# Optimization experiments

Hardware: AMD Instinct MI355X
Metric: run time of the kernel (lower is better)

Reference implementation:

```python
import jax, jax.numpy as jnp
import numpy as np

N_NODES = 100000
N_EDGES = 1000000

def _gcn_conv(x, W, b, src, dst, n_nodes):
    # PyG GCNConv: linear first, then symmetric-normalized aggregation with self loops
    x = x @ W  # [N, F_out]
    loop = jnp.arange(n_nodes, dtype=src.dtype)
    src2 = jnp.concatenate([src, loop])
    dst2 = jnp.concatenate([dst, loop])
    deg = jax.ops.segment_sum(jnp.ones(src2.shape[0], x.dtype), dst2, num_segments=n_nodes)
    dinv = jnp.where(deg > 0, jax.lax.rsqrt(deg), 0.0)
    norm = dinv[src2] * dinv[dst2]  # [E+N]
    msgs = x[src2] * norm[:, None]  # gather + scale
    out = jax.ops.segment_sum(msgs, dst2, num_segments=n_nodes)  # scatter-add
    return out + b

def _pair_norm_si(x):
    # mode 'PN-SI', scale=1
    x = x - x.mean(axis=0)
    row_norm = jnp.sqrt(1e-6 + jnp.sum(x * x, axis=1, keepdims=True))
    return x / row_norm

def setup_inputs() -> dict:
    key = jax.random.key(0)
    k1, k2, k3, k4 = jax.random.split(key, 4)
    in_c, hid_c, out_c = 256, 64, 40
    x = jax.random.normal(k1, (N_NODES, in_c), dtype=jnp.float32)
    edge_index = jax.random.randint(k2, (2, N_EDGES), 0, N_NODES, dtype=jnp.int64)
    W1 = jax.random.normal(k3, (in_c, hid_c), dtype=jnp.float32) / np.sqrt(in_c)
    b1 = jnp.zeros((hid_c,), jnp.float32)
    W2 = jax.random.normal(k4, (hid_c, out_c), dtype=jnp.float32) / np.sqrt(hid_c)
    b2 = jnp.zeros((out_c,), jnp.float32)
    return {"x": x, "edge_index": edge_index, "W1": W1, "b1": b1, "W2": W2, "b2": b2}

def reference(x, edge_index, W1, b1, W2, b2):
    src, dst = edge_index[0], edge_index[1]
    n = x.shape[0]
    h = jax.nn.relu(_gcn_conv(x, W1, b1, src, dst, n))
    h = _gcn_conv(h, W2, b2, src, dst, n)
    h = _pair_norm_si(h)
    return jax.nn.log_softmax(h, axis=1)
```

## Files before the change

### kernel.cpp

```cpp
#include <hip/hip_runtime.h>
#include <hip/hip_fp16.h>
#include <math.h>

#define F_IN  256
#define F_HID 64
#define F_OUT 40
#define HS2_LD 64

typedef _Float16 h8 __attribute__((ext_vector_type(8)));
typedef _Float16 h4 __attribute__((ext_vector_type(4)));
typedef float f4 __attribute__((ext_vector_type(4)));

__global__ void k_deg(const int* __restrict__ dst, unsigned* __restrict__ degc, int E) {
    int i = blockIdx.x * blockDim.x + threadIdx.x;
    if (i < E) atomicAdd(&degc[dst[i]], 1u);
}

__global__ __launch_bounds__(256) void k_scanA(const unsigned* __restrict__ degc,
                                               unsigned* __restrict__ exscan,
                                               unsigned* __restrict__ bsum, int N) {
    __shared__ unsigned s[256];
    int tid = threadIdx.x;
    int i = blockIdx.x * 256 + tid;
    unsigned v = (i < N) ? degc[i] : 0u;
    s[tid] = v;
    __syncthreads();
    for (int off = 1; off < 256; off <<= 1) {
        unsigned t = (tid >= off) ? s[tid - off] : 0u;
        __syncthreads();
        s[tid] += t;
        __syncthreads();
    }
    if (i < N) exscan[i] = s[tid] - v;
    if (tid == 255) bsum[blockIdx.x] = s[255];
}

__global__ __launch_bounds__(512) void k_scanB(unsigned* __restrict__ bsum, int nb) {
    __shared__ unsigned s[512];
    int tid = threadIdx.x;
    unsigned v = (tid < nb) ? bsum[tid] : 0u;
    s[tid] = v;
    __syncthreads();
    for (int off = 1; off < 512; off <<= 1) {
        unsigned t = (tid >= off) ? s[tid - off] : 0u;
        __syncthreads();
        s[tid] += t;
        __syncthreads();
    }
    if (tid < nb) bsum[tid] = s[tid] - v;
}

__global__ void k_scanC(const unsigned* __restrict__ degc, const unsigned* __restrict__ exscan,
                        const unsigned* __restrict__ bsum, unsigned* __restrict__ rowptr,
                        float* __restrict__ dinv, int N, int E) {
    int i = blockIdx.x * blockDim.x + threadIdx.x;
    if (i < N) {
        rowptr[i] = exscan[i] + bsum[i >> 8];
        dinv[i] = rsqrtf((float)degc[i] + 1.0f);
        if (i == 0) rowptr[N] = (unsigned)E;
    }
}

__global__ void k_fill(const int* __restrict__ src, const int* __restrict__ dst,
                       const unsigned* __restrict__ rowptr, unsigned* __restrict__ cursor,
                       unsigned* __restrict__ col, int E) {
    int e = blockIdx.x * blockDim.x + threadIdx.x;
    if (e >= E) return;
    int d = dst[e];
    unsigned p = atomicAdd(&cursor[d], 1u);
    col[rowptr[d] + p] = (unsigned)src[e];
}

__global__ void k_wt(const float* __restrict__ W1, __half* __restrict__ Wt) {
    int i = blockIdx.x * 256 + threadIdx.x;
    int k = i >> 6, n = i & 63;
    Wt[n * 256 + k] = __float2half(W1[i]);
}

#define XS 136
__global__ __launch_bounds__(256) void k_mm1(const float* __restrict__ x,
                                             const __half* __restrict__ Wth,
                                             const float* __restrict__ dinv,
                                             __half* __restrict__ hs1o, int N) {
    __shared__ _Float16 sX[64 * XS];
    const _Float16* Wt = (const _Float16*)Wth;
    _Float16* hs1 = (_Float16*)hs1o;
    int tid = threadIdx.x;
    int lane = tid & 63;
    int wv = tid >> 6;
    int m15 = lane & 15;
    int q = lane >> 4;
    int nbase = blockIdx.x * 64;

    h8 bf[8];
    #pragma unroll
    for (int kt = 0; kt < 8; ++kt)
        bf[kt] = *(const h8*)(Wt + (wv * 16 + m15) * 256 + kt * 32 + q * 8);

    f4 acc[4];
    #pragma unroll
    for (int mt = 0; mt < 4; ++mt) acc[mt] = (f4){0.f, 0.f, 0.f, 0.f};

    #pragma unroll
    for (int c = 0; c < 2; ++c) {
        #pragma unroll
        for (int p = 0; p < 8; ++p) {
            int idx = p * 256 + tid;
            int row = idx >> 5;
            int c4  = idx & 31;
            int node = nbase + row;
            float4 v = (node < N) ? *(const float4*)(x + (size_t)node * F_IN + c * 128 + c4 * 4)
                                  : make_float4(0.f, 0.f, 0.f, 0.f);
            h4 hv = { (_Float16)v.x, (_Float16)v.y, (_Float16)v.z, (_Float16)v.w };
            *(h4*)&sX[row * XS + c4 * 4] = hv;
        }
        __syncthreads();
        #pragma unroll
        for (int kt2 = 0; kt2 < 4; ++kt2) {
            #pragma unroll
            for (int mt = 0; mt < 4; ++mt) {
                h8 a = *(const h8*)&sX[(mt * 16 + m15) * XS + kt2 * 32 + q * 8];
                acc[mt] = __builtin_amdgcn_mfma_f32_16x16x32_f16(a, bf[c * 4 + kt2], acc[mt], 0, 0, 0);
            }
        }
        __syncthreads();
    }

    #pragma unroll
    for (int mt = 0; mt < 4; ++mt) {
        #pragma unroll
        for (int r = 0; r < 4; ++r) {
            int node = nbase + mt * 16 + q * 4 + r;
            if (node < N) {
                float din = dinv[node];
                hs1[(size_t)node * F_HID + wv * 16 + m15] = (_Float16)(acc[mt][r] * din);
            }
        }
    }
}

__global__ __launch_bounds__(256) void k_agg1(const unsigned* __restrict__ rowptr,
                                              const unsigned* __restrict__ col,
                                              const float* __restrict__ dinv,
                                              const __half* __restrict__ hs1,
                                              const float* __restrict__ bias1,
                                              float* __restrict__ agg1, int N) {
    int lane = threadIdx.x & 63;
    int w = blockIdx.x * 4 + (threadIdx.x >> 6);
    int na = 2 * w, nb = 2 * w + 1;
    if (na >= N) return;

    float dinA = dinv[na];
    unsigned aE = rowptr[na], aEnd = rowptr[na + 1];
    float accA = __half2float(hs1[(size_t)na * F_HID + lane]);

    bool hasB = (nb < N);
    float dinB = 0.f, accB = 0.f;
    unsigned bE = 0, bEnd = 0;
    if (hasB) {
        dinB = dinv[nb];
        bE = rowptr[nb]; bEnd = rowptr[nb + 1];
        accB = __half2float(hs1[(size_t)nb * F_HID + lane]);
    }

    while (aE + 4 <= aEnd && bE + 4 <= bEnd) {
        unsigned sa0 = col[aE], sa1 = col[aE + 1], sa2 = col[aE + 2], sa3 = col[aE + 3];
        unsigned sb0 = col[bE], sb1 = col[bE + 1], sb2 = col[bE + 2], sb3 = col[bE + 3];
        float va0 = __half2float(hs1[(size_t)sa0 * F_HID + lane]);
        float va1 = __half2float(hs1[(size_t)sa1 * F_HID + lane]);
        float va2 = __half2float(hs1[(size_t)sa2 * F_HID + lane]);
        float va3 = __half2float(hs1[(size_t)sa3 * F_HID + lane]);
        float vb0 = __half2float(hs1[(size_t)sb0 * F_HID + lane]);
        float vb1 = __half2float(hs1[(size_t)sb1 * F_HID + lane]);
        float vb2 = __half2float(hs1[(size_t)sb2 * F_HID + lane]);
        float vb3 = __half2float(hs1[(size_t)sb3 * F_HID + lane]);
        accA += (va0 + va1) + (va2 + va3);
        accB += (vb0 + vb1) + (vb2 + vb3);
        aE += 4; bE += 4;
    }
    while (aE + 4 <= aEnd) {
        unsigned s0 = col[aE], s1 = col[aE + 1], s2 = col[aE + 2], s3 = col[aE + 3];
        float v0 = __half2float(hs1[(size_t)s0 * F_HID + lane]);
        float v1 = __half2float(hs1[(size_t)s1 * F_HID + lane]);
        float v2 = __half2float(hs1[(size_t)s2 * F_HID + lane]);
        float v3 = __half2float(hs1[(size_t)s3 * F_HID + lane]);
        accA += (v0 + v1) + (v2 + v3);
        aE += 4;
    }
    while (bE + 4 <= bEnd) {
        unsigned s0 = col[bE], s1 = col[bE + 1], s2 = col[bE + 2], s3 = col[bE + 3];
        float v0 = __half2float(hs1[(size_t)s0 * F_HID + lane]);
        float v1 = __half2float(hs1[(size_t)s1 * F_HID + lane]);
        float v2 = __half2float(hs1[(size_t)s2 * F_HID + lane]);
        float v3 = __half2float(hs1[(size_t)s3 * F_HID + lane]);
        accB += (v0 + v1) + (v2 + v3);
        bE += 4;
    }
    while (aE < aEnd && bE < bEnd) {
        unsigned sa = col[aE], sb = col[bE];
        accA += __half2float(hs1[(size_t)sa * F_HID + lane]);
        accB += __half2float(hs1[(size_t)sb * F_HID + lane]);
        ++aE; ++bE;
    }
    while (aE < aEnd) { accA += __half2float(hs1[(size_t)col[aE] * F_HID + lane]); ++aE; }
    while (bE < bEnd) { accB += __half2float(hs1[(size_t)col[bE] * F_HID + lane]); ++bE; }

    float bv = bias1[lane];
    float vA = accA * dinA + bv;
    agg1[(size_t)na * F_HID + lane] = vA > 0.f ? vA : 0.f;
    if (hasB) {
        float vB = accB * dinB + bv;
        agg1[(size_t)nb * F_HID + lane] = vB > 0.f ? vB : 0.f;
    }
}

__global__ __launch_bounds__(320) void k_mm2(const float* __restrict__ a,
                                             const float* __restrict__ W2,
                                             const float* __restrict__ dinv,
                                             __half* __restrict__ hs2, int N) {
    __shared__ float sW[F_HID * F_OUT];
    int tid = threadIdx.x;
    for (int idx = tid; idx < F_HID * F_OUT; idx += 320) sW[idx] = W2[idx];
    __syncthreads();

    int f = tid % F_OUT, r = tid / F_OUT;
    int node = blockIdx.x * 8 + r;
    if (node >= N) return;
    const float* ar = a + (size_t)node * F_HID;
    float acc = 0.f;
    #pragma unroll 8
    for (int k = 0; k < F_HID; ++k) acc = fmaf(ar[k], sW[k * F_OUT + f], acc);
    hs2[(size_t)node * HS2_LD + f] = __float2half(acc * dinv[node]);
}

__global__ __launch_bounds__(256) void k_agg2(const unsigned* __restrict__ rowptr,
                                              const unsigned* __restrict__ col,
                                              const float* __restrict__ dinv,
                                              const __half* __restrict__ hs2,
                                              float* __restrict__ out,
                                              float* __restrict__ colsum, int N) {
    __shared__ float part[256];
    int lane = threadIdx.x & 63;
    int wid = threadIdx.x >> 6;
    int nwaves = gridDim.x * 4;
    float cacc = 0.f;
    if (lane < F_OUT) {
        for (int w = blockIdx.x * 4 + wid; 2 * w < N; w += nwaves) {
            int na = 2 * w, nb = 2 * w + 1;
            float dinA = dinv[na];
            unsigned aE = rowptr[na], aEnd = rowptr[na + 1];
            float accA = __half2float(hs2[(size_t)na * HS2_LD + lane]);
            bool hasB = (nb < N);
            float dinB = 0.f, accB = 0.f;
            unsigned bE = 0, bEnd = 0;
            if (hasB) {
                dinB = dinv[nb];
                bE = rowptr[nb]; bEnd = rowptr[nb + 1];
                accB = __half2float(hs2[(size_t)nb * HS2_LD + lane]);
            }

            while (aE + 4 <= aEnd && bE + 4 <= bEnd) {
                unsigned sa0 = col[aE], sa1 = col[aE + 1], sa2 = col[aE + 2], sa3 = col[aE + 3];
                unsigned sb0 = col[bE], sb1 = col[bE + 1], sb2 = col[bE + 2], sb3 = col[bE + 3];
                float va0 = __half2float(hs2[(size_t)sa0 * HS2_LD + lane]);
                float va1 = __half2float(hs2[(size_t)sa1 * HS2_LD + lane]);
                float va2 = __half2float(hs2[(size_t)sa2 * HS2_LD + lane]);
                float va3 = __half2float(hs2[(size_t)sa3 * HS2_LD + lane]);
                float vb0 = __half2float(hs2[(size_t)sb0 * HS2_LD + lane]);
                float vb1 = __half2float(hs2[(size_t)sb1 * HS2_LD + lane]);
                float vb2 = __half2float(hs2[(size_t)sb2 * HS2_LD + lane]);
                float vb3 = __half2float(hs2[(size_t)sb3 * HS2_LD + lane]);
                accA += (va0 + va1) + (va2 + va3);
                accB += (vb0 + vb1) + (vb2 + vb3);
                aE += 4; bE += 4;
            }
            while (aE + 4 <= aEnd) {
                unsigned s0 = col[aE], s1 = col[aE + 1], s2 = col[aE + 2], s3 = col[aE + 3];
                float v0 = __half2float(hs2[(size_t)s0 * HS2_LD + lane]);
                float v1 = __half2float(hs2[(size_t)s1 * HS2_LD + lane]);
                float v2 = __half2float(hs2[(size_t)s2 * HS2_LD + lane]);
                float v3 = __half2float(hs2[(size_t)s3 * HS2_LD + lane]);
                accA += (v0 + v1) + (v2 + v3);
                aE += 4;
            }
            while (bE + 4 <= bEnd) {
                unsigned s0 = col[bE], s1 = col[bE + 1], s2 = col[bE + 2], s3 = col[bE + 3];
                float v0 = __half2float(hs2[(size_t)s0 * HS2_LD + lane]);
                float v1 = __half2float(hs2[(size_t)s1 * HS2_LD + lane]);
                float v2 = __half2float(hs2[(size_t)s2 * HS2_LD + lane]);
                float v3 = __half2float(hs2[(size_t)s3 * HS2_LD + lane]);
                accB += (v0 + v1) + (v2 + v3);
                bE += 4;
            }
            while (aE < aEnd && bE < bEnd) {
                unsigned sa = col[aE], sb = col[bE];
                accA += __half2float(hs2[(size_t)sa * HS2_LD + lane]);
                accB += __half2float(hs2[(size_t)sb * HS2_LD + lane]);
                ++aE; ++bE;
            }
            while (aE < aEnd) { accA += __half2float(hs2[(size_t)col[aE] * HS2_LD + lane]); ++aE; }
            while (bE < bEnd) { accB += __half2float(hs2[(size_t)col[bE] * HS2_LD + lane]); ++bE; }

            accA *= dinA;
            out[(size_t)na * F_OUT + lane] = accA;
            cacc += accA;
            if (hasB) {
                accB *= dinB;
                out[(size_t)nb * F_OUT + lane] = accB;
                cacc += accB;
            }
        }
    }
    part[threadIdx.x] = cacc;
    __syncthreads();
    if (threadIdx.x < F_OUT) {
        float s = part[threadIdx.x] + part[64 + threadIdx.x] + part[128 + threadIdx.x] + part[192 + threadIdx.x];
        atomicAdd(&colsum[threadIdx.x], s);
    }
}

__global__ __launch_bounds__(128) void k_final(float* __restrict__ out,
                                               const float* __restrict__ colsum, int N) {
    __shared__ float sMean[F_OUT];
    if (threadIdx.x < F_OUT) sMean[threadIdx.x] = colsum[threadIdx.x] * (1.0f / (float)N);
    __syncthreads();
    int n = blockIdx.x * blockDim.x + threadIdx.x;
    if (n >= N) return;
    float* row = out + (size_t)n * F_OUT;
    float v[F_OUT];
    float ss = 0.f;
    #pragma unroll
    for (int f = 0; f < F_OUT; ++f) {
        float t = row[f] - sMean[f];
        v[f] = t;
        ss += t * t;
    }
    float scale = 1.0f / sqrtf(ss + 1e-6f);
    float m = -1e30f;
    #pragma unroll
    for (int f = 0; f < F_OUT; ++f) {
        float y = v[f] * scale;
        v[f] = y;
        m = fmaxf(m, y);
    }
    float sum = 0.f;
    #pragma unroll
    for (int f = 0; f < F_OUT; ++f) sum += expf(v[f] - m);
    float lse = logf(sum);
    #pragma unroll
    for (int f = 0; f < F_OUT; ++f) row[f] = v[f] - m - lse;
}

extern "C" void kernel_launch(void* const* d_in, const int* in_sizes, int n_in,
                              void* d_out, int out_size, void* d_ws, size_t ws_size,
                              hipStream_t stream) {
    const float* x  = (const float*)d_in[0];
    const int*   ei = (const int*)d_in[1];
    const float* W1 = (const float*)d_in[2];
    const float* b1 = (const float*)d_in[3];
    const float* W2 = (const float*)d_in[4];
    float* out = (float*)d_out;

    int N = in_sizes[0] / F_IN;
    int E = in_sizes[1] / 2;
    const int* src = ei;
    const int* dst = ei + E;

    unsigned* degc   = (unsigned*)d_ws;
    unsigned* cursor = degc + N;
    float*    colsum = (float*)(cursor + N);
    unsigned* rowptr = (unsigned*)(colsum + 64);
    unsigned* col    = rowptr + N + 1;
    float*    dinv   = (float*)(col + E);
    float*    agg1   = dinv + N;
    __half*   hs1    = (__half*)(agg1 + (size_t)64 * N);
    __half*   hs2    = hs1 + (size_t)64 * N;
    __half*   Wt     = hs2 + (size_t)64 * N;
    unsigned* exscan = (unsigned*)agg1;
    unsigned* bsum   = exscan + N;

    hipMemsetAsync(d_ws, 0, ((size_t)2 * N + 64) * sizeof(float), stream);

    int nA = (N + 255) / 256;
    k_deg<<<(E + 255) / 256, 256, 0, stream>>>(dst, degc, E);
    k_scanA<<<nA, 256, 0, stream>>>(degc, exscan, bsum, N);
    k_scanB<<<1, 512, 0, stream>>>(bsum, nA);
    k_scanC<<<nA, 256, 0, stream>>>(degc, exscan, bsum, rowptr, dinv, N, E);
    k_fill<<<(E + 255) / 256, 256, 0, stream>>>(src, dst, rowptr, cursor, col, E);
    k_wt<<<64, 256, 0, stream>>>(W1, Wt);
    k_mm1<<<(N + 63) / 64, 256, 0, stream>>>(x, Wt, dinv, hs1, N);
    int waves1 = (N + 1) / 2;
    k_agg1<<<(waves1 + 3) / 4, 256, 0, stream>>>(rowptr, col, dinv, hs1, b1, agg1, N);
    k_mm2<<<(N + 7) / 8, 320, 0, stream>>>(agg1, W2, dinv, hs2, N);
    k_agg2<<<2048, 256, 0, stream>>>(rowptr, col, dinv, hs2, out, colsum, N);
    k_final<<<(N + 127) / 128, 128, 0, stream>>>(out, colsum, N);
}
```

Baseline: 443.5 us.

## Pad CSR rows to multiples of eight and gather eight edges per wave

Each node's neighbour list now holds its real edges, then the node itself as an explicit self-loop, then padding up to a multiple of 8 that points at a dummy row N. The dummy row is scaled by 1 in the first matmul and forced to zero in the second. Both aggregation kernels then have each group of 8 lanes handle one edge with 16-byte fp16 vector loads, so one wave covers 8 edges per step and sums across groups with xor shuffles. This removes the scalar per-lane gathers and the ragged tail loops. The cost is an extra padding kernel, more column-index entries and wasted gathers on padding slots. Correctness also depends on dummy row N of the first-layer features being zero.

```diff
diff --git a/kernel.cpp b/kernel.cpp
--- a/kernel.cpp
+++ b/kernel.cpp
@@ -22,7 +22,7 @@
     __shared__ unsigned s[256];
     int tid = threadIdx.x;
     int i = blockIdx.x * 256 + tid;
-    unsigned v = (i < N) ? degc[i] : 0u;
+    unsigned v = (i < N) ? ((degc[i] + 8u) & ~7u) : 0u;
     s[tid] = v;
     __syncthreads();
     for (int off = 1; off < 256; off <<= 1) {
@@ -52,23 +52,36 @@
 
 __global__ void k_scanC(const unsigned* __restrict__ degc, const unsigned* __restrict__ exscan,
                         const unsigned* __restrict__ bsum, unsigned* __restrict__ rowptr,
-                        float* __restrict__ dinv, int N, int E) {
+                        float* __restrict__ dinv, int N) {
     int i = blockIdx.x * blockDim.x + threadIdx.x;
     if (i < N) {
-        rowptr[i] = exscan[i] + bsum[i >> 8];
+        unsigned rp = exscan[i] + bsum[i >> 8];
+        rowptr[i] = rp;
         dinv[i] = rsqrtf((float)degc[i] + 1.0f);
-        if (i == 0) rowptr[N] = (unsigned)E;
+        if (i == N - 1) rowptr[N] = rp + ((degc[i] + 8u) & ~7u);
+        if (i == 0) dinv[N] = 1.0f;
     }
 }
 
 __global__ void k_fill(const int* __restrict__ src, const int* __restrict__ dst,
                        const unsigned* __restrict__ rowptr, unsigned* __restrict__ cursor,
-                       unsigned* __restrict__ col, int E) {
+                       unsigned* __restrict__ colp, int E) {
     int e = blockIdx.x * blockDim.x + threadIdx.x;
     if (e >= E) return;
     int d = dst[e];
     unsigned p = atomicAdd(&cursor[d], 1u);
-    col[rowptr[d] + p] = (unsigned)src[e];
+    colp[rowptr[d] + p] = (unsigned)src[e];
+}
+
+__global__ void k_pad(const unsigned* __restrict__ degc, const unsigned* __restrict__ rowptr,
+                      unsigned* __restrict__ colp, int N) {
+    int i = blockIdx.x * blockDim.x + threadIdx.x;
+    if (i >= N) return;
+    unsigned d = degc[i];
+    unsigned base = rowptr[i];
+    unsigned pd = (d + 8u) & ~7u;
+    colp[base + d] = (unsigned)i;
+    for (unsigned p = d + 1; p < pd; ++p) colp[base + p] = (unsigned)N;
 }
 
 __global__ void k_wt(const float* __restrict__ W1, __half* __restrict__ Wt) {
@@ -131,8 +144,8 @@
         #pragma unroll
         for (int r = 0; r < 4; ++r) {
             int node = nbase + mt * 16 + q * 4 + r;
-            if (node < N) {
-                float din = dinv[node];
+            if (node <= N) {
+                float din = (node < N) ? dinv[node] : 1.0f;
                 hs1[(size_t)node * F_HID + wv * 16 + m15] = (_Float16)(acc[mt][r] * din);
             }
         }
@@ -140,182 +153,200 @@
 }
 
 __global__ __launch_bounds__(256) void k_agg1(const unsigned* __restrict__ rowptr,
-                                              const unsigned* __restrict__ col,
+                                              const unsigned* __restrict__ colp,
                                               const float* __restrict__ dinv,
-                                              const __half* __restrict__ hs1,
+                                              const __half* __restrict__ hs1o,
                                               const float* __restrict__ bias1,
                                               float* __restrict__ agg1, int N) {
+    const _Float16* hp = (const _Float16*)hs1o;
     int lane = threadIdx.x & 63;
     int w = blockIdx.x * 4 + (threadIdx.x >> 6);
     int na = 2 * w, nb = 2 * w + 1;
     if (na >= N) return;
-
-    float dinA = dinv[na];
+    int g = lane >> 3, c = lane & 7;
+
+    float accA[8], accB[8];
+    #pragma unroll
+    for (int j = 0; j < 8; ++j) { accA[j] = 0.f; accB[j] = 0.f; }
+
     unsigned aE = rowptr[na], aEnd = rowptr[na + 1];
-    float accA = __half2float(hs1[(size_t)na * F_HID + lane]);
-
     bool hasB = (nb < N);
-    float dinB = 0.f, accB = 0.f;
     unsigned bE = 0, bEnd = 0;
-    if (hasB) {
-        dinB = dinv[nb];
-        bE = rowptr[nb]; bEnd = rowptr[nb + 1];
-        accB = __half2float(hs1[(size_t)nb * F_HID + lane]);
-    }
-
-    while (aE + 4 <= aEnd && bE + 4 <= bEnd) {
-        unsigned sa0 = col[aE], sa1 = col[aE + 1], sa2 = col[aE + 2], sa3 = col[aE + 3];
-        unsigned sb0 = col[bE], sb1 = col[bE + 1], sb2 = col[bE + 2], sb3 = col[bE + 3];
-        float va0 = __half2float(hs1[(size_t)sa0 * F_HID + lane]);
-        float va1 = __half2float(hs1[(size_t)sa1 * F_HID + lane]);
-        float va2 = __half2float(hs1[(size_t)sa2 * F_HID + lane]);
-        float va3 = __half2float(hs1[(size_t)sa3 * F_HID + lane]);
-        float vb0 = __half2float(hs1[(size_t)sb0 * F_HID + lane]);
-        float vb1 = __half2float(hs1[(size_t)sb1 * F_HID + lane]);
-        float vb2 = __half2float(hs1[(size_t)sb2 * F_HID + lane]);
-        float vb3 = __half2float(hs1[(size_t)sb3 * F_HID + lane]);
-        accA += (va0 + va1) + (va2 + va3);
-        accB += (vb0 + vb1) + (vb2 + vb3);
-        aE += 4; bE += 4;
-    }
-    while (aE + 4 <= aEnd) {
-        unsigned s0 = col[aE], s1 = col[aE + 1], s2 = col[aE + 2], s3 = col[aE + 3];
-        float v0 = __half2float(hs1[(size_t)s0 * F_HID + lane]);
-        float v1 = __half2float(hs1[(size_t)s1 * F_HID + lane]);
-        float v2 = __half2float(hs1[(size_t)s2 * F_HID + lane]);
-        float v3 = __half2float(hs1[(size_t)s3 * F_HID + lane]);
-        accA += (v0 + v1) + (v2 + v3);
-        aE += 4;
-    }
-    while (bE + 4 <= bEnd) {
-        unsigned s0 = col[bE], s1 = col[bE + 1], s2 = col[bE + 2], s3 = col[bE + 3];
-        float v0 = __half2float(hs1[(size_t)s0 * F_HID + lane]);
-        float v1 = __half2float(hs1[(size_t)s1 * F_HID + lane]);
-        float v2 = __half2float(hs1[(size_t)s2 * F_HID + lane]);
-        float v3 = __half2float(hs1[(size_t)s3 * F_HID + lane]);
-        accB += (v0 + v1) + (v2 + v3);
-        bE += 4;
-    }
+    if (hasB) { bE = rowptr[nb]; bEnd = rowptr[nb + 1]; }
+
     while (aE < aEnd && bE < bEnd) {
-        unsigned sa = col[aE], sb = col[bE];
-        accA += __half2float(hs1[(size_t)sa * F_HID + lane]);
-        accB += __half2float(hs1[(size_t)sb * F_HID + lane]);
-        ++aE; ++bE;
-    }
-    while (aE < aEnd) { accA += __half2float(hs1[(size_t)col[aE] * F_HID + lane]); ++aE; }
-    while (bE < bEnd) { accB += __half2float(hs1[(size_t)col[bE] * F_HID + lane]); ++bE; }
-
-    float bv = bias1[lane];
-    float vA = accA * dinA + bv;
-    agg1[(size_t)na * F_HID + lane] = vA > 0.f ? vA : 0.f;
-    if (hasB) {
-        float vB = accB * dinB + bv;
-        agg1[(size_t)nb * F_HID + lane] = vB > 0.f ? vB : 0.f;
-    }
-}
-
-__global__ __launch_bounds__(320) void k_mm2(const float* __restrict__ a,
+        unsigned sA = colp[aE + g];
+        unsigned sB = colp[bE + g];
+        h8 va = *(const h8*)(hp + (size_t)sA * F_HID + c * 8);
+        h8 vb = *(const h8*)(hp + (size_t)sB * F_HID + c * 8);
+        #pragma unroll
+        for (int j = 0; j < 8; ++j) { accA[j] += (float)va[j]; accB[j] += (float)vb[j]; }
+        aE += 8; bE += 8;
+    }
+    while (aE < aEnd) {
+        unsigned sA = colp[aE + g];
+        h8 va = *(const h8*)(hp + (size_t)sA * F_HID + c * 8);
+        #pragma unroll
+        for (int j = 0; j < 8; ++j) accA[j] += (float)va[j];
+        aE += 8;
+    }
+    while (bE < bEnd) {
+        unsigned sB = colp[bE + g];
+        h8 vb = *(const h8*)(hp + (size_t)sB * F_HID + c * 8);
+        #pragma unroll
+        for (int j = 0; j < 8; ++j) accB[j] += (float)vb[j];
+        bE += 8;
+    }
+
+    #pragma unroll
+    for (int off = 8; off <= 32; off <<= 1) {
+        #pragma unroll
+        for (int j = 0; j < 8; ++j) {
+            accA[j] += __shfl_xor(accA[j], off, 64);
+            accB[j] += __shfl_xor(accB[j], off, 64);
+        }
+    }
+
+    if (g == 0) {
+        float4 b0 = *(const float4*)(bias1 + c * 8);
+        float4 b1v = *(const float4*)(bias1 + c * 8 + 4);
+        float dinA = dinv[na];
+        float4 o0, o1;
+        o0.x = fmaxf(accA[0] * dinA + b0.x, 0.f); o0.y = fmaxf(accA[1] * dinA + b0.y, 0.f);
+        o0.z = fmaxf(accA[2] * dinA + b0.z, 0.f); o0.w = fmaxf(accA[3] * dinA + b0.w, 0.f);
+        o1.x = fmaxf(accA[4] * dinA + b1v.x, 0.f); o1.y = fmaxf(accA[5] * dinA + b1v.y, 0.f);
+        o1.z = fmaxf(accA[6] * dinA + b1v.z, 0.f); o1.w = fmaxf(accA[7] * dinA + b1v.w, 0.f);
+        *(float4*)(agg1 + (size_t)na * F_HID + c * 8) = o0;
+        *(float4*)(agg1 + (size_t)na * F_HID + c * 8 + 4) = o1;
+        if (hasB) {
+            float dinB = dinv[nb];
+            o0.x = fmaxf(accB[0] * dinB + b0.x, 0.f); o0.y = fmaxf(accB[1] * dinB + b0.y, 0.f);
+            o0.z = fmaxf(accB[2] * dinB + b0.z, 0.f); o0.w = fmaxf(accB[3] * dinB + b0.w, 0.f);
+            o1.x = fmaxf(accB[4] * dinB + b1v.x, 0.f); o1.y = fmaxf(accB[5] * dinB + b1v.y, 0.f);
+            o1.z = fmaxf(accB[6] * dinB + b1v.z, 0.f); o1.w = fmaxf(accB[7] * dinB + b1v.w, 0.f);
+            *(float4*)(agg1 + (size_t)nb * F_HID + c * 8) = o0;
+            *(float4*)(agg1 + (size_t)nb * F_HID + c * 8 + 4) = o1;
+        }
+    }
+}
+
+__global__ __launch_bounds__(512) void k_mm2(const float* __restrict__ a,
                                              const float* __restrict__ W2,
                                              const float* __restrict__ dinv,
                                              __half* __restrict__ hs2, int N) {
-    __shared__ float sW[F_HID * F_OUT];
+    __shared__ float sW[F_HID * 64];
     int tid = threadIdx.x;
-    for (int idx = tid; idx < F_HID * F_OUT; idx += 320) sW[idx] = W2[idx];
+    for (int idx = tid; idx < F_HID * 64; idx += 512) {
+        int k = idx >> 6, f = idx & 63;
+        sW[idx] = (f < F_OUT) ? W2[k * F_OUT + f] : 0.f;
+    }
     __syncthreads();
 
-    int f = tid % F_OUT, r = tid / F_OUT;
+    int f = tid & 63, r = tid >> 6;
     int node = blockIdx.x * 8 + r;
-    if (node >= N) return;
+    if (node > N) return;
     const float* ar = a + (size_t)node * F_HID;
     float acc = 0.f;
     #pragma unroll 8
-    for (int k = 0; k < F_HID; ++k) acc = fmaf(ar[k], sW[k * F_OUT + f], acc);
-    hs2[(size_t)node * HS2_LD + f] = __float2half(acc * dinv[node]);
+    for (int k = 0; k < F_HID; ++k) acc = fmaf(ar[k], sW[k * 64 + f], acc);
+    float val = (node < N) ? acc * dinv[node] : 0.f;
+    hs2[(size_t)node * HS2_LD + f] = __float2half(val);
 }
 
 __global__ __launch_bounds__(256) void k_agg2(const unsigned* __restrict__ rowptr,
-                                              const unsigned* __restrict__ col,
+                                              const unsigned* __restrict__ colp,
                                               const float* __restrict__ dinv,
-                                              const __half* __restrict__ hs2,
+                                              const __half* __restrict__ hs2o,
                                               float* __restrict__ out,
                                               float* __restrict__ colsum, int N) {
-    __shared__ float part[256];
+    __shared__ float part[4][8][8];
+    const _Float16* hp = (const _Float16*)hs2o;
     int lane = threadIdx.x & 63;
-    int wid = threadIdx.x >> 6;
+    int wv = threadIdx.x >> 6;
+    int g = lane >> 3, c = lane & 7;
     int nwaves = gridDim.x * 4;
-    float cacc = 0.f;
-    if (lane < F_OUT) {
-        for (int w = blockIdx.x * 4 + wid; 2 * w < N; w += nwaves) {
-            int na = 2 * w, nb = 2 * w + 1;
+    float csum[8];
+    #pragma unroll
+    for (int j = 0; j < 8; ++j) csum[j] = 0.f;
+
+    for (int w = blockIdx.x * 4 + wv; 2 * w < N; w += nwaves) {
+        int na = 2 * w, nb = 2 * w + 1;
+        float accA[8], accB[8];
+        #pragma unroll
+        for (int j = 0; j < 8; ++j) { accA[j] = 0.f; accB[j] = 0.f; }
+
+        unsigned aE = rowptr[na], aEnd = rowptr[na + 1];
+        bool hasB = (nb < N);
+        unsigned bE = 0, bEnd = 0;
+        if (hasB) { bE = rowptr[nb]; bEnd = rowptr[nb + 1]; }
+
+        while (aE < aEnd && bE < bEnd) {
+            unsigned sA = colp[aE + g];
+            unsigned sB = colp[bE + g];
+            h8 va = *(const h8*)(hp + (size_t)sA * HS2_LD + c * 8);
+            h8 vb = *(const h8*)(hp + (size_t)sB * HS2_LD + c * 8);
+            #pragma unroll
+            for (int j = 0; j < 8; ++j) { accA[j] += (float)va[j]; accB[j] += (float)vb[j]; }
+            aE += 8; bE += 8;
+        }
+        while (aE < aEnd) {
+            unsigned sA = colp[aE + g];
+            h8 va = *(const h8*)(hp + (size_t)sA * HS2_LD + c * 8);
+            #pragma unroll
+            for (int j = 0; j < 8; ++j) accA[j] += (float)va[j];
+            aE += 8;
+        }
+        while (bE < bEnd) {
+            unsigned sB = colp[bE + g];
+            h8 vb = *(const h8*)(hp + (size_t)sB * HS2_LD + c * 8);
+            #pragma unroll
+            for (int j = 0; j < 8; ++j) accB[j] += (float)vb[j];
+            bE += 8;
+        }
+
+        #pragma unroll
+        for (int off = 8; off <= 32; off <<= 1) {
+            #pragma unroll
+            for (int j = 0; j < 8; ++j) {
+                accA[j] += __shfl_xor(accA[j], off, 64);
+                accB[j] += __shfl_xor(accB[j], off, 64);
+            }
+        }
+
+        if (g == 0) {
             float dinA = dinv[na];
-            unsigned aE = rowptr[na], aEnd = rowptr[na + 1];
-            float accA = __half2float(hs2[(size_t)na * HS2_LD + lane]);
-            bool hasB = (nb < N);
-            float dinB = 0.f, accB = 0.f;
-            unsigned bE = 0, bEnd = 0;
+            #pragma unroll
+            for (int j = 0; j < 8; ++j) { accA[j] *= dinA; csum[j] += accA[j]; }
+            if (c < 5) {
+                *(float4*)(out + (size_t)na * F_OUT + c * 8) =
+                    make_float4(accA[0], accA[1], accA[2], accA[3]);
+                *(float4*)(out + (size_t)na * F_OUT + c * 8 + 4) =
+                    make_float4(accA[4], accA[5], accA[6], accA[7]);
+            }
             if (hasB) {
-                dinB = dinv[nb];
-                bE = rowptr[nb]; bEnd = rowptr[nb + 1];
-                accB = __half2float(hs2[(size_t)nb * HS2_LD + lane]);
+                float dinB = dinv[nb];
+                #pragma unroll
+                for (int j = 0; j < 8; ++j) { accB[j] *= dinB; csum[j] += accB[j]; }
+                if (c < 5) {
+                    *(float4*)(out + (size_t)nb * F_OUT + c * 8) =
+                        make_float4(accB[0], accB[1], accB[2], accB[3]);
+                    *(float4*)(out + (size_t)nb * F_OUT + c * 8 + 4) =
+                        make_float4(accB[4], accB[5], accB[6], accB[7]);
+                }
             }
-
-            while (aE + 4 <= aEnd && bE + 4 <= bEnd) {
-                unsigned sa0 = col[aE], sa1 = col[aE + 1], sa2 = col[aE + 2], sa3 = col[aE + 3];
-                unsigned sb0 = col[bE], sb1 = col[bE + 1], sb2 = col[bE + 2], sb3 = col[bE + 3];
-                float va0 = __half2float(hs2[(size_t)sa0 * HS2_LD + lane]);
-                float va1 = __half2float(hs2[(size_t)sa1 * HS2_LD + lane]);
-                float va2 = __half2float(hs2[(size_t)sa2 * HS2_LD + lane]);
-                float va3 = __half2float(hs2[(size_t)sa3 * HS2_LD + lane]);
-                float vb0 = __half2float(hs2[(size_t)sb0 * HS2_LD + lane]);
-                float vb1 = __half2float(hs2[(size_t)sb1 * HS2_LD + lane]);
-                float vb2 = __half2float(hs2[(size_t)sb2 * HS2_LD + lane]);
-                float vb3 = __half2float(hs2[(size_t)sb3 * HS2_LD + lane]);
-                accA += (va0 + va1) + (va2 + va3);
-                accB += (vb0 + vb1) + (vb2 + vb3);
-                aE += 4; bE += 4;
-            }
-            while (aE + 4 <= aEnd) {
-                unsigned s0 = col[aE], s1 = col[aE + 1], s2 = col[aE + 2], s3 = col[aE + 3];
-                float v0 = __half2float(hs2[(size_t)s0 * HS2_LD + lane]);
-                float v1 = __half2float(hs2[(size_t)s1 * HS2_LD + lane]);
-                float v2 = __half2float(hs2[(size_t)s2 * HS2_LD + lane]);
-                float v3 = __half2float(hs2[(size_t)s3 * HS2_LD + lane]);
-                accA += (v0 + v1) + (v2 + v3);
-                aE += 4;
-            }
-            while (bE + 4 <= bEnd) {
-                unsigned s0 = col[bE], s1 = col[bE + 1], s2 = col[bE + 2], s3 = col[bE + 3];
-                float v0 = __half2float(hs2[(size_t)s0 * HS2_LD + lane]);
-                float v1 = __half2float(hs2[(size_t)s1 * HS2_LD + lane]);
-                float v2 = __half2float(hs2[(size_t)s2 * HS2_LD + lane]);
-                float v3 = __half2float(hs2[(size_t)s3 * HS2_LD + lane]);
-                accB += (v0 + v1) + (v2 + v3);
-                bE += 4;
-            }
-            while (aE < aEnd && bE < bEnd) {
-                unsigned sa = col[aE], sb = col[bE];
-                accA += __half2float(hs2[(size_t)sa * HS2_LD + lane]);
-                accB += __half2float(hs2[(size_t)sb * HS2_LD + lane]);
-                ++aE; ++bE;
-            }
-            while (aE < aEnd) { accA += __half2float(hs2[(size_t)col[aE] * HS2_LD + lane]); ++aE; }
-            while (bE < bEnd) { accB += __half2float(hs2[(size_t)col[bE] * HS2_LD + lane]); ++bE; }
-
-            accA *= dinA;
-            out[(size_t)na * F_OUT + lane] = accA;
-            cacc += accA;
-            if (hasB) {
-                accB *= dinB;
-                out[(size_t)nb * F_OUT + lane] = accB;
-                cacc += accB;
-            }
-        }
-    }
-    part[threadIdx.x] = cacc;
+        }
+    }
+
+    if (g == 0) {
+        #pragma unroll
+        for (int j = 0; j < 8; ++j) part[wv][c][j] = csum[j];
+    }
     __syncthreads();
-    if (threadIdx.x < F_OUT) {
-        float s = part[threadIdx.x] + part[64 + threadIdx.x] + part[128 + threadIdx.x] + part[192 + threadIdx.x];
-        atomicAdd(&colsum[threadIdx.x], s);
+    int tid = threadIdx.x;
+    if (tid < F_OUT) {
+        int cc = tid >> 3, jj = tid & 7;
+        float s = part[0][cc][jj] + part[1][cc][jj] + part[2][cc][jj] + part[3][cc][jj];
+        atomicAdd(&colsum[tid], s);
     }
 }
 
@@ -366,32 +397,35 @@
     const int* src = ei;
     const int* dst = ei + E;
 
-    unsigned* degc   = (unsigned*)d_ws;
-    unsigned* cursor = degc + N;
-    float*    colsum = (float*)(cursor + N);
-    unsigned* rowptr = (unsigned*)(colsum + 64);
-    unsigned* col    = rowptr + N + 1;
-    float*    dinv   = (float*)(col + E);
-    float*    agg1   = dinv + N;
-    __half*   hs1    = (__half*)(agg1 + (size_t)64 * N);
-    __half*   hs2    = hs1 + (size_t)64 * N;
-    __half*   Wt     = hs2 + (size_t)64 * N;
+    char* p = (char*)d_ws;
+    auto alloc = [&](size_t bytes) { char* r = p; p += (bytes + 127) & ~(size_t)127; return r; };
+    unsigned* degc   = (unsigned*)alloc((size_t)N * 4);
+    unsigned* cursor = (unsigned*)alloc((size_t)N * 4);
+    float*    colsum = (float*)   alloc(64 * 4);
+    unsigned* rowptr = (unsigned*)alloc((size_t)(N + 1) * 4);
+    unsigned* colp   = (unsigned*)alloc((size_t)(E + 8 * N + 8) * 4);
+    float*    dinv   = (float*)   alloc((size_t)(N + 1) * 4);
+    float*    agg1   = (float*)   alloc((size_t)64 * (N + 1) * 4);
+    __half*   hs1    = (__half*)  alloc((size_t)64 * (N + 1) * 2);
+    __half*   hs2    = (__half*)  alloc((size_t)64 * (N + 1) * 2);
+    __half*   Wt     = (__half*)  alloc((size_t)16384 * 2);
     unsigned* exscan = (unsigned*)agg1;
     unsigned* bsum   = exscan + N;
 
-    hipMemsetAsync(d_ws, 0, ((size_t)2 * N + 64) * sizeof(float), stream);
+    hipMemsetAsync(d_ws, 0, (char*)(colsum + 64) - (char*)d_ws, stream);
 
     int nA = (N + 255) / 256;
     k_deg<<<(E + 255) / 256, 256, 0, stream>>>(dst, degc, E);
     k_scanA<<<nA, 256, 0, stream>>>(degc, exscan, bsum, N);
     k_scanB<<<1, 512, 0, stream>>>(bsum, nA);
-    k_scanC<<<nA, 256, 0, stream>>>(degc, exscan, bsum, rowptr, dinv, N, E);
-    k_fill<<<(E + 255) / 256, 256, 0, stream>>>(src, dst, rowptr, cursor, col, E);
+    k_scanC<<<nA, 256, 0, stream>>>(degc, exscan, bsum, rowptr, dinv, N);
+    k_fill<<<(E + 255) / 256, 256, 0, stream>>>(src, dst, rowptr, cursor, colp, E);
+    k_pad<<<nA, 256, 0, stream>>>(degc, rowptr, colp, N);
     k_wt<<<64, 256, 0, stream>>>(W1, Wt);
     k_mm1<<<(N + 63) / 64, 256, 0, stream>>>(x, Wt, dinv, hs1, N);
     int waves1 = (N + 1) / 2;
-    k_agg1<<<(waves1 + 3) / 4, 256, 0, stream>>>(rowptr, col, dinv, hs1, b1, agg1, N);
-    k_mm2<<<(N + 7) / 8, 320, 0, stream>>>(agg1, W2, dinv, hs2, N);
-    k_agg2<<<2048, 256, 0, stream>>>(rowptr, col, dinv, hs2, out, colsum, N);
+    k_agg1<<<(waves1 + 3) / 4, 256, 0, stream>>>(rowptr, colp, dinv, hs1, b1, agg1, N);
+    k_mm2<<<(N + 8) / 8, 512, 0, stream>>>(agg1, W2, dinv, hs2, N);
+    k_agg2<<<2048, 256, 0, stream>>>(rowptr, colp, dinv, hs2, out, colsum, N);
     k_final<<<(N + 127) / 128, 128, 0, stream>>>(out, colsum, N);
 }
```

After: 461.9 us. 1.04x slower.
